# Kernel optimization log

Measured on AMD Instinct MI355X. Metric: run time of the kernel, lower is better.

Reference implementation:

```python
import jax, jax.numpy as jnp
import numpy as np
from jax import lax

B, H, W_IN, C = 32, 32, 32, 128   # NHWC input
KH, KW = 3, 3                     # kernel size (padding 'same', stride 1)
F = 512                           # filters


def setup_inputs() -> dict:
    key = jax.random.key(0)
    ks = jax.random.split(key, 10)
    # sparse factor shapes: (KH*KW*C, 1152), (1152, F), (F, F)
    d0, d1, d2, d3 = KH * KW * C, 1152, F, F
    x = jax.random.normal(ks[0], (B, H, W_IN, C), dtype=jnp.float32)
    k0 = jax.random.normal(ks[1], (d0, d1), dtype=jnp.float32) * (1.0 / np.sqrt(d0))
    k1 = jax.random.normal(ks[2], (d1, d2), dtype=jnp.float32) * (1.0 / np.sqrt(d1))
    k2 = jax.random.normal(ks[3], (d2, d3), dtype=jnp.float32) * (1.0 / np.sqrt(d2))
    # fixed binary sparsity masks (K.constant in the original build)
    m0 = jax.random.bernoulli(ks[4], 0.1, (d0, d1)).astype(jnp.float32)
    m1 = jax.random.bernoulli(ks[5], 0.1, (d1, d2)).astype(jnp.float32)
    m2 = jax.random.bernoulli(ks[6], 0.1, (d2, d3)).astype(jnp.float32)
    scale = jax.random.normal(ks[7], (1,), dtype=jnp.float32)
    bias = jax.random.normal(ks[8], (F,), dtype=jnp.float32) * 0.01
    return {"x": x, "k0": k0, "k1": k1, "k2": k2,
            "m0": m0, "m1": m1, "m2": m2, "scale": scale, "bias": bias}


def reference(x, k0, k1, k2, m0, m1, m2, scale, bias):
    # Chained masked sparse factors collapse (associativity) to one effective
    # filter matrix of shape (KH*KW*C, F); the im2col row flatten order in the
    # original is (h, w, c), which matches an HWIO reshape exactly.
    w_eff = (k0 * m0) @ (k1 * m1) @ (k2 * m2)          # (KH*KW*C, F)
    w = (w_eff * scale[0]).reshape(KH, KW, C, F)        # fold scalar scale into kernel
    out = lax.conv_general_dilated(
        x, w, window_strides=(1, 1), padding='SAME',
        dimension_numbers=('NHWC', 'HWIO', 'NHWC'))     # (B, H, W, F)
    return out + bias
```

## Files before the change

kernel.cpp:

```cpp
#include <hip/hip_runtime.h>

typedef __attribute__((ext_vector_type(8))) short short8;
typedef __attribute__((ext_vector_type(4))) float f32x4;

typedef __attribute__((address_space(1))) const unsigned gas_u32;
typedef __attribute__((address_space(3))) unsigned las_u32;

static __device__ __forceinline__ void g2l16(const void* g, void* l) {
  __builtin_amdgcn_global_load_lds((gas_u32*)g, (las_u32*)l, 16, 0, 0);
}

static __device__ __forceinline__ short f2bf(float f) {
  union { float f; unsigned u; } v; v.f = f;
  unsigned r = (v.u + 0x7FFFu + ((v.u >> 16) & 1u)) >> 16;
  return (short)r;
}

static __device__ __forceinline__ void xcvt_body(const float* __restrict__ x,
                                                 short* __restrict__ xbp, int i) {
  int c8 = i & 15;
  int t = i >> 4;
  int wp = t % 34, t2 = t / 34;
  int hp = t2 % 34, b = t2 / 34;
  short8 o = {};
  if (hp >= 1 && hp <= 32 && wp >= 1 && wp <= 32) {
    const f32x4* s = (const f32x4*)(x + (((size_t)((b << 5) + hp - 1) << 5) + (wp - 1)) * 128 + c8 * 8);
    f32x4 a = s[0], bb2 = s[1];
    o[0] = f2bf(a[0]); o[1] = f2bf(a[1]); o[2] = f2bf(a[2]); o[3] = f2bf(a[3]);
    o[4] = f2bf(bb2[0]); o[5] = f2bf(bb2[1]); o[6] = f2bf(bb2[2]); o[7] = f2bf(bb2[3]);
  }
  ((short8*)xbp)[i] = o;
}

__global__ __launch_bounds__(256) void k_prepw(const float* __restrict__ k0f,
                                               const float* __restrict__ m0f,
                                               const float* __restrict__ scf,
                                               const float* __restrict__ k1f,
                                               const float* __restrict__ m1f,
                                               const float* __restrict__ k2f,
                                               const float* __restrict__ m2f,
                                               short* __restrict__ w1b,
                                               short* __restrict__ w2T,
                                               short* __restrict__ w3T) {
  __shared__ float tile[32][33];
  const int bb = blockIdx.x, tid = threadIdx.x;
  if (bb < 648) {
    int i = bb * 256 + tid;
    float s = scf[0];
    const f32x4* kk = (const f32x4*)k0f + (size_t)i * 2;
    const f32x4* mm = (const f32x4*)m0f + (size_t)i * 2;
    f32x4 a0 = kk[0], a1 = kk[1], b0 = mm[0], b1 = mm[1];
    short8 o;
    o[0] = f2bf(a0[0] * b0[0] * s); o[1] = f2bf(a0[1] * b0[1] * s);
    o[2] = f2bf(a0[2] * b0[2] * s); o[3] = f2bf(a0[3] * b0[3] * s);
    o[4] = f2bf(a1[0] * b1[0] * s); o[5] = f2bf(a1[1] * b1[1] * s);
    o[6] = f2bf(a1[2] * b1[2] * s); o[7] = f2bf(a1[3] * b1[3] * s);
    ((short8*)w1b)[i] = o;
  } else {
    const float *kf, *mf; short* outp; int D, F, idx;
    if (bb < 1224) { kf = k1f; mf = m1f; outp = w2T; D = 1152; F = 512; idx = bb - 648; }
    else           { kf = k2f; mf = m2f; outp = w3T; D = 512;  F = 512; idx = bb - 1224; }
    int f0 = (idx & 15) * 32, d0 = (idx >> 4) * 32;
    int tx = tid & 31, ty = tid >> 5;
#pragma unroll
    for (int i = 0; i < 4; ++i) {
      int d = d0 + ty + i * 8;
      size_t ix = (size_t)d * F + f0 + tx;
      tile[ty + i * 8][tx] = kf[ix] * mf[ix];
    }
    __syncthreads();
#pragma unroll
    for (int i = 0; i < 4; ++i) {
      int f = f0 + ty + i * 8;
      outp[(size_t)f * D + d0 + tx] = f2bf(tile[tx][ty + i * 8]);
    }
  }
}

__global__ __launch_bounds__(256) void k_gemm64x(const short* __restrict__ A,
                                                 const short* __restrict__ BT,
                                                 short* __restrict__ C, int M, int N, int K,
                                                 const float* __restrict__ x,
                                                 short* __restrict__ xbp, int xoff) {
  __shared__ __align__(16) short As[64][64];
  __shared__ __align__(16) short Bs[64][64];
  if (blockIdx.x >= 144) {
    xcvt_body(x, xbp, (xoff + (int)blockIdx.x - 144) * 256 + (int)threadIdx.x);
    return;
  }
  const int ntiles = N >> 6;
  const int m0 = (blockIdx.x / ntiles) << 6, n0 = (blockIdx.x % ntiles) << 6;
  const int tid = threadIdx.x;
  const int lane = tid & 63, wv = tid >> 6;
  const int wr = (wv >> 1) * 32, wc = (wv & 1) * 32;
  const int lr = lane & 15, lk = (lane >> 4) * 8;

  f32x4 acc[2][2] = {};

  const int rr = tid >> 3, c8 = (tid & 7) * 8;
  unsigned abase[2], bbase[2];
#pragma unroll
  for (int j = 0; j < 2; ++j) {
    abase[j] = (unsigned)(m0 + j * 32 + rr) * K + c8;
    bbase[j] = (unsigned)(n0 + j * 32 + rr) * K + c8;
  }
  short* AsL = &As[0][0];
  short* BsL = &Bs[0][0];
  const int lo = wv * 512;

  for (int kt = 0; kt < K; kt += 64) {
#pragma unroll
    for (int j = 0; j < 2; ++j) g2l16(A + abase[j] + kt, AsL + j * 2048 + lo);
#pragma unroll
    for (int j = 0; j < 2; ++j) g2l16(BT + bbase[j] + kt, BsL + j * 2048 + lo);
    __syncthreads();
#pragma unroll
    for (int ks = 0; ks < 2; ++ks) {
      const int ko = ks * 32 + lk;
      short8 af[2], bf[2];
#pragma unroll
      for (int i = 0; i < 2; ++i) af[i] = *(const short8*)&As[wr + i * 16 + lr][ko];
#pragma unroll
      for (int i = 0; i < 2; ++i) bf[i] = *(const short8*)&Bs[wc + i * 16 + lr][ko];
#pragma unroll
      for (int mi = 0; mi < 2; ++mi)
#pragma unroll
        for (int ni = 0; ni < 2; ++ni)
          acc[mi][ni] = __builtin_amdgcn_mfma_f32_16x16x32_bf16(af[mi], bf[ni], acc[mi][ni], 0, 0, 0);
    }
    __syncthreads();
  }
#pragma unroll
  for (int mi = 0; mi < 2; ++mi) {
    const int row = m0 + wr + mi * 16 + (lane >> 4) * 4;
#pragma unroll
    for (int ni = 0; ni < 2; ++ni) {
      const int col = n0 + wc + ni * 16 + lr;
#pragma unroll
      for (int q = 0; q < 4; ++q)
        C[(size_t)(row + q) * N + col] = f2bf(acc[mi][ni][q]);
    }
  }
}

#define MF(a_, b_, c_) __builtin_amdgcn_mfma_f32_16x16x32_bf16(a_, b_, c_, 0, 0, 0)

#define RD_A(mf_, ks_) \
  (*(const short8*)&As[wr * 128 + (mf_) * 16 + lr][(((ks_) * 4 + lh) ^ (lr & 7)) * 8])
#define RD_B(nf_, ks_) \
  (*(const short8*)&Bs[wc * 32 + (nf_) * 16 + lr][(((ks_) * 4 + lh) ^ (lr & 7)) * 8])

#define LOADB do { \
  bfr[0][0] = RD_B(0, 0); bfr[0][1] = RD_B(0, 1); \
  bfr[1][0] = RD_B(1, 0); bfr[1][1] = RD_B(1, 1); } while (0)

#define STAGE_AQ(q_, tt_) do { \
  const int tc_ = (tt_) > 17 ? 17 : (tt_); \
  const int khw_ = tc_ >> 1; const int kh_ = (khw_ * 11) >> 5; const int kw_ = khw_ - kh_ * 3; \
  const int ao_ = (kh_ * 34 + kw_) * 128 + ((tc_ & 1) << 6) + (q_) * 4352; \
  g2l16(xbp + aBase + ao_, &As[aRow + (q_) * 32][0]); } while (0)

#define STAGE_BH(j_, tt_) do { \
  const int tc_ = (tt_) > 17 ? 17 : (tt_); \
  g2l16(wT + bBase + (j_) * 73728 + tc_ * 64, &Bs[(j_) * 64 + bRow][0]); } while (0)

#define MFMA8(p_) \
  acc[2*(p_)  ][0] = MF(a0k0, bfr[0][0], acc[2*(p_)  ][0]); \
  acc[2*(p_)  ][1] = MF(a0k0, bfr[1][0], acc[2*(p_)  ][1]); \
  acc[2*(p_)+1][0] = MF(a1k0, bfr[0][0], acc[2*(p_)+1][0]); \
  acc[2*(p_)+1][1] = MF(a1k0, bfr[1][0], acc[2*(p_)+1][1]); \
  acc[2*(p_)  ][0] = MF(a0k1, bfr[0][1], acc[2*(p_)  ][0]); \
  acc[2*(p_)  ][1] = MF(a0k1, bfr[1][1], acc[2*(p_)  ][1]); \
  acc[2*(p_)+1][0] = MF(a1k1, bfr[0][1], acc[2*(p_)+1][0]); \
  acc[2*(p_)+1][1] = MF(a1k1, bfr[1][1], acc[2*(p_)+1][1]);

#define PHASE(p_, PRE, WAITV, ...) do { \
  PRE; \
  short8 a0k0 = RD_A(2*(p_), 0),   a0k1 = RD_A(2*(p_), 1); \
  short8 a1k0 = RD_A(2*(p_)+1, 0), a1k1 = RD_A(2*(p_)+1, 1); \
  __builtin_amdgcn_s_barrier(); \
  asm volatile("s_waitcnt lgkmcnt(0)" ::: "memory"); \
  __builtin_amdgcn_sched_barrier(0); \
  __VA_ARGS__ \
  __builtin_amdgcn_s_setprio(1); \
  MFMA8(p_) \
  __builtin_amdgcn_s_setprio(0); \
  WAITV; \
  __builtin_amdgcn_s_barrier(); \
} while (0)

#define VM5 asm volatile("s_waitcnt vmcnt(5)" ::: "memory")
#define VM3 asm volatile("s_waitcnt vmcnt(3)" ::: "memory")

__global__ __launch_bounds__(512, 4) void k_conv(const short* __restrict__ xbp,
                                                 const short* __restrict__ wT,
                                                 const float* __restrict__ bias,
                                                 float* __restrict__ out) {
  __shared__ __align__(16) short As[256][64];
  __shared__ __align__(16) short Bs[128][64];
  int bid = blockIdx.x;
  bid = (bid & 7) * 64 + (bid >> 3);
  const int mt = bid >> 2, nt = bid & 3;
  const int m0 = mt << 8, n0 = nt << 7;
  const int tid = threadIdx.x;
  const int lane = tid & 63, wid = tid >> 6;
  const int wr = wid >> 2, wc = wid & 3;
  const int lr = lane & 15, lh = lane >> 4;

  f32x4 acc[8][2] = {};
  short8 bfr[2][2];

  const int wrB = (wid >> 2) * 128;
  const int rsub = (wid & 3) * 8 + (lane >> 3);
  const int sw = (lane & 7) ^ (lane >> 3);
  const int aRow = wrB + (wid & 3) * 8;
  const int bRow = wid * 8;

  const int Mb = m0 + wrB + rsub;
  const int b = Mb >> 10, h0 = (Mb >> 5) & 31, w = Mb & 31;
  const unsigned aBase = (unsigned)((b * 34 + h0) * 34 + w) * 128 + sw * 8;
  const unsigned bBase = (unsigned)(n0 + wid * 8 + (lane >> 3)) * 1152 + sw * 8;

  STAGE_BH(0, 0); STAGE_BH(1, 0);
  STAGE_AQ(0, 0); STAGE_AQ(1, 0); STAGE_AQ(2, 0); STAGE_AQ(3, 0);
  asm volatile("s_waitcnt vmcnt(0)" ::: "memory");
  __builtin_amdgcn_s_barrier();

  for (int t = 0; t < 18; ++t) {
    const int tn = t + 1;
    PHASE(0, LOADB, VM5, STAGE_BH(0, tn); STAGE_BH(1, tn); STAGE_AQ(0, tn););
    PHASE(1, ,      VM5, STAGE_AQ(1, tn););
    PHASE(2, ,      VM5, STAGE_AQ(2, tn););
    PHASE(3, ,      VM3, STAGE_AQ(3, tn););
  }
  asm volatile("s_waitcnt vmcnt(0)" ::: "memory");

  const int orow = m0 + wr * 128, ocol = n0 + wc * 32;
#pragma unroll
  for (int mf = 0; mf < 8; ++mf) {
    const int row = orow + mf * 16 + lh * 4;
#pragma unroll
    for (int nf = 0; nf < 2; ++nf) {
      const int col = ocol + nf * 16 + lr;
      const float bv = bias[col];
#pragma unroll
      for (int q = 0; q < 4; ++q)
        out[(size_t)(row + q) * 512 + col] = acc[mf][nf][q] + bv;
    }
  }
}

extern "C" void kernel_launch(void* const* d_in, const int* in_sizes, int n_in,
                              void* d_out, int out_size, void* d_ws, size_t ws_size,
                              hipStream_t stream) {
  (void)in_sizes; (void)n_in; (void)out_size; (void)ws_size;
  const float* x    = (const float*)d_in[0];
  const float* k0   = (const float*)d_in[1];
  const float* k1   = (const float*)d_in[2];
  const float* k2   = (const float*)d_in[3];
  const float* m0   = (const float*)d_in[4];
  const float* m1   = (const float*)d_in[5];
  const float* m2   = (const float*)d_in[6];
  const float* sc   = (const float*)d_in[7];
  const float* bias = (const float*)d_in[8];
  float* out = (float*)d_out;
  char* ws = (char*)d_ws;

  short* xbp = (short*)(ws);
  short* w1b = (short*)(ws + 9469952);
  short* w2T = (short*)(ws + 12124160);
  short* w3T = (short*)(ws + 13303808);
  short* A1b = (short*)(ws + 13828096);
  short* wET = (short*)(ws + 15007744);

  k_prepw<<<1480, 256, 0, stream>>>(k0, m0, sc, k1, m1, k2, m2, w1b, w2T, w3T);
  k_gemm64x<<<1300, 256, 0, stream>>>(w1b, w2T, A1b, 1152, 512, 1152, x, xbp, 0);
  k_gemm64x<<<1300, 256, 0, stream>>>(w3T, A1b, wET, 512, 1152, 512, x, xbp, 1156);
  k_conv<<<512, 512, 0, stream>>>(xbp, wET, bias, out);
}
```

Before: 76.42 us.

## Double-buffer weight-chain GEMM with 128-wide K tiles and swizzled LDS

Rewrites the small weight-product GEMM to use double-buffered LDS tiles with a K step of 128 instead of 64. The next tile's global-to-LDS load is issued before computing on the current one. The LDS layout is XOR-swizzled to avoid bank conflicts on the MFMA fragment reads. This halves the barrier count and overlaps load latency with compute, at the cost of four times the LDS per block, which may reduce occupancy.

```diff
diff --git a/kernel.cpp b/kernel.cpp
--- a/kernel.cpp
+++ b/kernel.cpp
@@ -15,6 +15,8 @@
   unsigned r = (v.u + 0x7FFFu + ((v.u >> 16) & 1u)) >> 16;
   return (short)r;
 }
+
+#define MF(a_, b_, c_) __builtin_amdgcn_mfma_f32_16x16x32_bf16(a_, b_, c_, 0, 0, 0)
 
 static __device__ __forceinline__ void xcvt_body(const float* __restrict__ x,
                                                  short* __restrict__ xbp, int i) {
@@ -77,13 +79,13 @@
   }
 }
 
-__global__ __launch_bounds__(256) void k_gemm64x(const short* __restrict__ A,
-                                                 const short* __restrict__ BT,
-                                                 short* __restrict__ C, int M, int N, int K,
-                                                 const float* __restrict__ x,
-                                                 short* __restrict__ xbp, int xoff) {
-  __shared__ __align__(16) short As[64][64];
-  __shared__ __align__(16) short Bs[64][64];
+__global__ __launch_bounds__(256) void k_gemmx(const short* __restrict__ A,
+                                               const short* __restrict__ BT,
+                                               short* __restrict__ C, int M, int N, int K,
+                                               const float* __restrict__ x,
+                                               short* __restrict__ xbp, int xoff) {
+  __shared__ __align__(16) short As[2][64][128];
+  __shared__ __align__(16) short Bs[2][64][128];
   if (blockIdx.x >= 144) {
     xcvt_body(x, xbp, (xoff + (int)blockIdx.x - 144) * 256 + (int)threadIdx.x);
     return;
@@ -93,46 +95,54 @@
   const int tid = threadIdx.x;
   const int lane = tid & 63, wv = tid >> 6;
   const int wr = (wv >> 1) * 32, wc = (wv & 1) * 32;
-  const int lr = lane & 15, lk = (lane >> 4) * 8;
+  const int lr = lane & 15, lh = lane >> 4;
+
+  const int rr = tid >> 4, sl = tid & 15;
+  const int swz = sl ^ (rr & 7);
+  const unsigned aOff = (unsigned)(m0 + rr) * K + swz * 8;
+  const unsigned bOff = (unsigned)(n0 + rr) * K + swz * 8;
+  const int ldsRow = 4 * wv;
 
   f32x4 acc[2][2] = {};
 
-  const int rr = tid >> 3, c8 = (tid & 7) * 8;
-  unsigned abase[2], bbase[2];
-#pragma unroll
-  for (int j = 0; j < 2; ++j) {
-    abase[j] = (unsigned)(m0 + j * 32 + rr) * K + c8;
-    bbase[j] = (unsigned)(n0 + j * 32 + rr) * K + c8;
-  }
-  short* AsL = &As[0][0];
-  short* BsL = &Bs[0][0];
-  const int lo = wv * 512;
-
-  for (int kt = 0; kt < K; kt += 64) {
-#pragma unroll
-    for (int j = 0; j < 2; ++j) g2l16(A + abase[j] + kt, AsL + j * 2048 + lo);
-#pragma unroll
-    for (int j = 0; j < 2; ++j) g2l16(BT + bbase[j] + kt, BsL + j * 2048 + lo);
-    __syncthreads();
-#pragma unroll
-    for (int ks = 0; ks < 2; ++ks) {
-      const int ko = ks * 32 + lk;
+#define GST(buf_, kt_) do { \
+    _Pragma("unroll") for (int j = 0; j < 4; ++j) \
+      g2l16(A + aOff + (unsigned)j * 16u * (unsigned)K + (unsigned)(kt_) * 128u, \
+            &As[buf_][j * 16 + ldsRow][0]); \
+    _Pragma("unroll") for (int j = 0; j < 4; ++j) \
+      g2l16(BT + bOff + (unsigned)j * 16u * (unsigned)K + (unsigned)(kt_) * 128u, \
+            &Bs[buf_][j * 16 + ldsRow][0]); \
+  } while (0)
+
+  const int nk = K >> 7;
+  GST(0, 0);
+  asm volatile("s_waitcnt vmcnt(0)" ::: "memory");
+  __builtin_amdgcn_s_barrier();
+
+  for (int kt = 0; kt < nk; ++kt) {
+    const int cur = kt & 1;
+    if (kt + 1 < nk) { if (cur) GST(0, kt + 1); else GST(1, kt + 1); }
+#pragma unroll
+    for (int ks = 0; ks < 4; ++ks) {
       short8 af[2], bf[2];
 #pragma unroll
-      for (int i = 0; i < 2; ++i) af[i] = *(const short8*)&As[wr + i * 16 + lr][ko];
-#pragma unroll
-      for (int i = 0; i < 2; ++i) bf[i] = *(const short8*)&Bs[wc + i * 16 + lr][ko];
+      for (int i = 0; i < 2; ++i)
+        af[i] = *(const short8*)&As[cur][wr + i * 16 + lr][((ks * 4 + lh) ^ (lr & 7)) * 8];
+#pragma unroll
+      for (int i = 0; i < 2; ++i)
+        bf[i] = *(const short8*)&Bs[cur][wc + i * 16 + lr][((ks * 4 + lh) ^ (lr & 7)) * 8];
 #pragma unroll
       for (int mi = 0; mi < 2; ++mi)
 #pragma unroll
         for (int ni = 0; ni < 2; ++ni)
-          acc[mi][ni] = __builtin_amdgcn_mfma_f32_16x16x32_bf16(af[mi], bf[ni], acc[mi][ni], 0, 0, 0);
-    }
-    __syncthreads();
+          acc[mi][ni] = MF(af[mi], bf[ni], acc[mi][ni]);
+    }
+    if (kt + 1 < nk) asm volatile("s_waitcnt vmcnt(0)" ::: "memory");
+    __builtin_amdgcn_s_barrier();
   }
 #pragma unroll
   for (int mi = 0; mi < 2; ++mi) {
-    const int row = m0 + wr + mi * 16 + (lane >> 4) * 4;
+    const int row = m0 + wr + mi * 16 + lh * 4;
 #pragma unroll
     for (int ni = 0; ni < 2; ++ni) {
       const int col = n0 + wc + ni * 16 + lr;
@@ -141,9 +151,8 @@
         C[(size_t)(row + q) * N + col] = f2bf(acc[mi][ni][q]);
     }
   }
-}
-
-#define MF(a_, b_, c_) __builtin_amdgcn_mfma_f32_16x16x32_bf16(a_, b_, c_, 0, 0, 0)
+#undef GST
+}
 
 #define RD_A(mf_, ks_) \
   (*(const short8*)&As[wr * 128 + (mf_) * 16 + lr][(((ks_) * 4 + lh) ^ (lr & 7)) * 8])
@@ -274,7 +283,7 @@
   short* wET = (short*)(ws + 15007744);
 
   k_prepw<<<1480, 256, 0, stream>>>(k0, m0, sc, k1, m1, k2, m2, w1b, w2T, w3T);
-  k_gemm64x<<<1300, 256, 0, stream>>>(w1b, w2T, A1b, 1152, 512, 1152, x, xbp, 0);
-  k_gemm64x<<<1300, 256, 0, stream>>>(w3T, A1b, wET, 512, 1152, 512, x, xbp, 1156);
+  k_gemmx<<<1300, 256, 0, stream>>>(w1b, w2T, A1b, 1152, 512, 1152, x, xbp, 0);
+  k_gemmx<<<1300, 256, 0, stream>>>(w3T, A1b, wET, 512, 1152, 512, x, xbp, 1156);
   k_conv<<<512, 512, 0, stream>>>(xbp, wET, bias, out);
 }
```

New measurement: 69.06 us. 1.11x faster.
